# Optimization experiments

Measured on AMD Instinct MI355X. Metric: run time of the kernel, lower is better.

## Reference

```python
import jax, jax.numpy as jnp
import numpy as np

B, N, D = 4, 4096, 1024
H = 16
DH = D // H  # 64
SCALE = DH ** 0.5


def setup_inputs() -> dict:
    key = jax.random.key(0)
    ks = jax.random.split(key, 10)
    bound = float(np.sqrt(6.0 / (D + D)))  # xavier_uniform for square weights
    lin_b = float(1.0 / np.sqrt(D))        # default nn.Linear bias init bound
    return {
        "q": jax.random.normal(ks[0], (B, N, D), dtype=jnp.float32),
        "k": jax.random.normal(ks[1], (B, N, D), dtype=jnp.float32),
        "v": jax.random.normal(ks[2], (B, N, D), dtype=jnp.float32),
        "Wq": jax.random.uniform(ks[3], (D, D), jnp.float32, -bound, bound),
        "bq": jax.random.uniform(ks[4], (D,), jnp.float32, -lin_b, lin_b),
        "Wk": jax.random.uniform(ks[5], (D, D), jnp.float32, -bound, bound),
        "bk": jax.random.uniform(ks[6], (D,), jnp.float32, -lin_b, lin_b),
        "Wv": jax.random.uniform(ks[7], (D, D), jnp.float32, -bound, bound),
        "bv": jax.random.uniform(ks[8], (D,), jnp.float32, -lin_b, lin_b),
        "Wo": jax.random.uniform(ks[9], (D, D), jnp.float32, -bound, bound),
    }


def _split_heads(x):
    # [b, n, h*d] -> [b, h, n, d]
    b, n, _ = x.shape
    return x.reshape(b, n, H, DH).transpose(0, 2, 1, 3)


def reference(q, k, v, Wq, bq, Wk, bk, Wv, bv, Wo):
    qp = _split_heads(q @ Wq.T + bq)  # [b,h,n,d]
    kp = _split_heads(k @ Wk.T + bk)
    vp = _split_heads(v @ Wv.T + bv)

    inv_qtr = SCALE ** (-0.25)
    qs = jax.nn.softmax(qp, axis=-1) * inv_qtr            # feature-wise softmax on Q
    ctx = jnp.einsum('bhnd,bhne->bhde', kp, vp)           # K^T V: [b,h,d,d]
    ctx = jax.nn.softmax(ctx, axis=-2) * inv_qtr          # softmax over first d axis
    att = jnp.einsum('bhnd,bhde->bhne', qs, ctx)          # [b,h,n,d]

    att = att.transpose(0, 2, 1, 3).reshape(q.shape[0], q.shape[1], D)  # b n (h d)
    return att @ Wo.T  # to_out linear (no bias); dropout p=0 -> identity
```

## Files before the change

kernel.cpp:

```cpp
#include <hip/hip_runtime.h>

#define INV_QTR 0.59460355750136053f

typedef _Float16 f16;
typedef _Float16 f16x8 __attribute__((ext_vector_type(8)));
typedef float f32x4 __attribute__((ext_vector_type(4)));

__device__ __forceinline__ f16x8 load_cvt8(const float* p) {
    const f32x4* q = (const f32x4*)p;
    f32x4 a = q[0], b = q[1];
    f16x8 r;
    #pragma unroll
    for (int j = 0; j < 4; ++j) { r[j] = (f16)a[j]; r[j + 4] = (f16)b[j]; }
    return r;
}

template <bool XF, bool OF, bool BIAS>
__device__ __forceinline__ void gemm_bt_body(const void* __restrict__ X,
                                             const float* __restrict__ W,
                                             const float* __restrict__ bias,
                                             void* __restrict__ dst) {
    __shared__ __align__(16) f16 As[128 * 64];
    __shared__ __align__(16) f16 Bs[128 * 64];

    const int tid  = threadIdx.x;
    const int lane = tid & 63;
    const int wave = tid >> 6;
    const int m0   = blockIdx.x * 128;
    const int n0   = blockIdx.y * 128;
    const int wm   = (wave >> 1) * 64;
    const int wn   = (wave & 1) * 64;
    const int frow = lane & 15;
    const int quad = lane >> 4;

    f32x4 acc[4][4] = {};

    for (int k0 = 0; k0 < 1024; k0 += 64) {
        f16x8 stA[4], stB[4];
        #pragma unroll
        for (int i = 0; i < 4; ++i) {
            int slot = i * 256 + tid;
            int row  = slot >> 3;
            int sc   = slot & 7;
            int gc   = sc ^ (row & 7);
            size_t ax = (size_t)(m0 + row) * 1024 + k0 + gc * 8;
            if (XF) stA[i] = load_cvt8((const float*)X + ax);
            else    stA[i] = *(const f16x8*)((const f16*)X + ax);
            stB[i] = load_cvt8(W + (size_t)(n0 + row) * 1024 + k0 + gc * 8);
        }
        __syncthreads();
        #pragma unroll
        for (int i = 0; i < 4; ++i) {
            int slot = i * 256 + tid;
            *(f16x8*)(As + slot * 8) = stA[i];
            *(f16x8*)(Bs + slot * 8) = stB[i];
        }
        __syncthreads();

        #pragma unroll
        for (int kk = 0; kk < 2; ++kk) {
            f16x8 fa[4], fb[4];
            #pragma unroll
            for (int t = 0; t < 4; ++t) {
                int arow = wm + t * 16 + frow;
                int asc  = (kk * 4 + quad) ^ (arow & 7);
                fa[t] = *(const f16x8*)(As + arow * 64 + asc * 8);
                int brow = wn + t * 16 + frow;
                int bsc  = (kk * 4 + quad) ^ (brow & 7);
                fb[t] = *(const f16x8*)(Bs + brow * 64 + bsc * 8);
            }
            #pragma unroll
            for (int tm = 0; tm < 4; ++tm)
                #pragma unroll
                for (int tn = 0; tn < 4; ++tn)
                    acc[tm][tn] = __builtin_amdgcn_mfma_f32_16x16x32_f16(
                        fa[tm], fb[tn], acc[tm][tn], 0, 0, 0);
        }
    }

    #pragma unroll
    for (int tn = 0; tn < 4; ++tn) {
        int col = n0 + wn + tn * 16 + frow;
        float badd = BIAS ? bias[col] : 0.0f;
        #pragma unroll
        for (int tm = 0; tm < 4; ++tm) {
            #pragma unroll
            for (int r = 0; r < 4; ++r) {
                size_t idx = (size_t)(m0 + wm + tm * 16 + quad * 4 + r) * 1024 + col;
                float v = acc[tm][tn][r] + badd;
                if (OF) ((float*)dst)[idx] = v;
                else    ((f16*)dst)[idx] = (f16)v;
            }
        }
    }
}

__global__ void qkv_gemm(const float* __restrict__ q, const float* __restrict__ k,
                         const float* __restrict__ v,
                         const float* __restrict__ Wq, const float* __restrict__ bq,
                         const float* __restrict__ Wk, const float* __restrict__ bk,
                         const float* __restrict__ Wv, const float* __restrict__ bv,
                         f16* __restrict__ qp, f16* __restrict__ kp,
                         f16* __restrict__ vp) {
    int z = blockIdx.z;
    const float* X = (z == 0) ? q : (z == 1) ? k : v;
    const float* W = (z == 0) ? Wq : (z == 1) ? Wk : Wv;
    const float* bias = (z == 0) ? bq : (z == 1) ? bk : bv;
    f16* dst = (z == 0) ? qp : (z == 1) ? kp : vp;
    gemm_bt_body<true, false, true>(X, W, bias, dst);
}

__global__ void out_gemm(const f16* __restrict__ att, const float* __restrict__ Wo,
                         float* __restrict__ out) {
    gemm_bt_body<false, true, false>(att, Wo, nullptr, out);
}

__global__ void q_softmax(f16* __restrict__ qp) {
    int gid  = blockIdx.x * 4 + (threadIdx.x >> 6);
    int lane = threadIdx.x & 63;
    size_t off = (size_t)gid * 64 + lane;
    float x = (float)qp[off];
    float m = x;
    #pragma unroll
    for (int s = 32; s; s >>= 1) m = fmaxf(m, __shfl_xor(m, s, 64));
    float e = __expf(x - m);
    float sum = e;
    #pragma unroll
    for (int s = 32; s; s >>= 1) sum += __shfl_xor(sum, s, 64);
    qp[off] = (f16)(e / sum * INV_QTR);
}

__global__ void ctx_partial(const f16* __restrict__ kp, const f16* __restrict__ vp,
                            float* __restrict__ part) {
    int slice = blockIdx.x, bh = blockIdx.y;
    int b = bh >> 4, h = bh & 15;
    int tid = threadIdx.x, lane = tid & 63, wave = tid >> 6;
    __shared__ __align__(16) f16 kS[64 * 64];
    __shared__ __align__(16) f16 vS[64 * 64];

    const size_t base = ((size_t)b * 4096 + slice * 512) * 1024 + h * 64;
    const int dg = wave * 16;
    float acc[16] = {};

    for (int c = 0; c < 8; ++c) {
        f16x8 sk[2], sv[2];
        #pragma unroll
        for (int i = 0; i < 2; ++i) {
            int slot = i * 256 + tid, row = slot >> 3, ch = slot & 7;
            size_t g = base + (size_t)(c * 64 + row) * 1024 + ch * 8;
            sk[i] = *(const f16x8*)(kp + g);
            sv[i] = *(const f16x8*)(vp + g);
        }
        __syncthreads();
        #pragma unroll
        for (int i = 0; i < 2; ++i) {
            int slot = i * 256 + tid;
            *(f16x8*)(kS + slot * 8) = sk[i];
            *(f16x8*)(vS + slot * 8) = sv[i];
        }
        __syncthreads();
        #pragma unroll 4
        for (int n = 0; n < 64; ++n) {
            float vv = (float)vS[n * 64 + lane];
            f16x8 k0 = *(const f16x8*)(kS + n * 64 + dg);
            f16x8 k1 = *(const f16x8*)(kS + n * 64 + dg + 8);
            #pragma unroll
            for (int j = 0; j < 8; ++j) {
                acc[j]     += (float)k0[j] * vv;
                acc[8 + j] += (float)k1[j] * vv;
            }
        }
    }
    float* dst = part + ((size_t)(slice * 64 + bh) * 64 + dg) * 64 + lane;
    #pragma unroll
    for (int j = 0; j < 16; ++j) dst[j * 64] = acc[j];
}

__global__ void ctx_softmax(const float* __restrict__ part, f16* __restrict__ ctxT) {
    int bh = blockIdx.x;
    int tid = threadIdx.x;
    __shared__ float cs[64 * 65];
    float a[16];
    #pragma unroll
    for (int j = 0; j < 16; ++j) a[j] = 0.f;
    for (int s = 0; s < 8; ++s) {
        const float* p = part + (size_t)(s * 64 + bh) * 4096;
        #pragma unroll
        for (int j = 0; j < 16; ++j) a[j] += p[j * 256 + tid];
    }
    #pragma unroll
    for (int j = 0; j < 16; ++j) {
        int f = j * 256 + tid;
        cs[(f >> 6) * 65 + (f & 63)] = a[j];
    }
    __syncthreads();
    int lane = tid & 63, wave = tid >> 6;
    #pragma unroll
    for (int i = 0; i < 16; ++i) {
        int e = wave * 16 + i;
        float x = cs[lane * 65 + e];
        float m = x;
        #pragma unroll
        for (int s2 = 32; s2; s2 >>= 1) m = fmaxf(m, __shfl_xor(m, s2, 64));
        float ex = __expf(x - m);
        float sum = ex;
        #pragma unroll
        for (int s2 = 32; s2; s2 >>= 1) sum += __shfl_xor(sum, s2, 64);
        ctxT[((size_t)bh * 64 + e) * 64 + lane] = (f16)(ex / sum * INV_QTR);
    }
}

__global__ void att_gemm(const f16* __restrict__ qs, const f16* __restrict__ ctxT,
                         f16* __restrict__ att) {
    __shared__ __align__(16) f16 As[2][128 * 64];
    __shared__ __align__(16) f16 Bs[2][64 * 64];
    int tid = threadIdx.x, lane = tid & 63, wave = tid >> 6;
    int m0 = blockIdx.x * 128;
    int n0 = blockIdx.y * 128;
    int b  = m0 >> 12;
    int h0 = (n0 >> 6) & 15;

    #pragma unroll
    for (int ch = 0; ch < 2; ++ch) {
        #pragma unroll
        for (int i = 0; i < 4; ++i) {
            int slot = i * 256 + tid, row = slot >> 3, sc = slot & 7, gc = sc ^ (row & 7);
            *(f16x8*)(As[ch] + slot * 8) =
                *(const f16x8*)(qs + (size_t)(m0 + row) * 1024 + n0 + ch * 64 + gc * 8);
        }
        #pragma unroll
        for (int i = 0; i < 2; ++i) {
            int slot = i * 256 + tid, row = slot >> 3, sc = slot & 7, gc = sc ^ (row & 7);
            int bh = b * 16 + h0 + ch;
            *(f16x8*)(Bs[ch] + slot * 8) =
                *(const f16x8*)(ctxT + ((size_t)bh * 64 + row) * 64 + gc * 8);
        }
    }
    __syncthreads();

    int wm = (wave >> 1) * 64, wn = wave & 1;
    int frow = lane & 15, quad = lane >> 4;
    f32x4 acc[4][4] = {};
    #pragma unroll
    for (int kk = 0; kk < 2; ++kk) {
        f16x8 fa[4], fb[4];
        #pragma unroll
        for (int t = 0; t < 4; ++t) {
            int arow = wm + t * 16 + frow;
            int asc  = (kk * 4 + quad) ^ (arow & 7);
            fa[t] = *(const f16x8*)(As[wn] + arow * 64 + asc * 8);
            int brow = t * 16 + frow;
            int bsc  = (kk * 4 + quad) ^ (brow & 7);
            fb[t] = *(const f16x8*)(Bs[wn] + brow * 64 + bsc * 8);
        }
        #pragma unroll
        for (int tm = 0; tm < 4; ++tm)
            #pragma unroll
            for (int tn = 0; tn < 4; ++tn)
                acc[tm][tn] = __builtin_amdgcn_mfma_f32_16x16x32_f16(
                    fa[tm], fb[tn], acc[tm][tn], 0, 0, 0);
    }
    #pragma unroll
    for (int tn = 0; tn < 4; ++tn) {
        int col = n0 + wn * 64 + tn * 16 + frow;
        #pragma unroll
        for (int tm = 0; tm < 4; ++tm) {
            #pragma unroll
            for (int r = 0; r < 4; ++r) {
                int row = m0 + wm + tm * 16 + quad * 4 + r;
                att[(size_t)row * 1024 + col] = (f16)acc[tm][tn][r];
            }
        }
    }
}

extern "C" void kernel_launch(void* const* d_in, const int* in_sizes, int n_in,
                              void* d_out, int out_size, void* d_ws, size_t ws_size,
                              hipStream_t stream) {
    const float* q  = (const float*)d_in[0];
    const float* k  = (const float*)d_in[1];
    const float* v  = (const float*)d_in[2];
    const float* Wq = (const float*)d_in[3];
    const float* bq = (const float*)d_in[4];
    const float* Wk = (const float*)d_in[5];
    const float* bk = (const float*)d_in[6];
    const float* Wv = (const float*)d_in[7];
    const float* bv = (const float*)d_in[8];
    const float* Wo = (const float*)d_in[9];

    char* ws = (char*)d_ws;
    f16*   qp   = (f16*)ws;
    f16*   kp   = (f16*)(ws + 33554432);
    float* part = (float*)(ws + 67108864);
    f16*   ctxT = (f16*)(ws + 75497472);
    f16*   vp   = (f16*)d_out;
    float* out  = (float*)d_out;

    qkv_gemm<<<dim3(128, 8, 3), 256, 0, stream>>>(q, k, v, Wq, bq, Wk, bk, Wv, bv,
                                                  qp, kp, vp);
    q_softmax<<<65536, 256, 0, stream>>>(qp);
    ctx_partial<<<dim3(8, 64), 256, 0, stream>>>(kp, vp, part);
    ctx_softmax<<<64, 256, 0, stream>>>(part, ctxT);
    att_gemm<<<dim3(128, 8), 256, 0, stream>>>(qp, ctxT, kp);
    out_gemm<<<dim3(128, 8), 256, 0, stream>>>(kp, Wo, out);
}
```

Before: 589.5 us.

## Pre-convert inputs and weights to fp16 and load GEMM tiles directly into LDS

```diff
diff --git a/kernel.cpp b/kernel.cpp
--- a/kernel.cpp
+++ b/kernel.cpp
@@ -6,20 +6,45 @@
 typedef _Float16 f16x8 __attribute__((ext_vector_type(8)));
 typedef float f32x4 __attribute__((ext_vector_type(4)));
 
-__device__ __forceinline__ f16x8 load_cvt8(const float* p) {
-    const f32x4* q = (const f32x4*)p;
-    f32x4 a = q[0], b = q[1];
+__device__ __forceinline__ void gload16(const void* g, void* l) {
+    __builtin_amdgcn_global_load_lds(
+        (const __attribute__((address_space(1))) void*)g,
+        (__attribute__((address_space(3))) void*)l, 16, 0, 0);
+}
+
+__global__ void cvt_all(const float* __restrict__ q, const float* __restrict__ k,
+                        const float* __restrict__ v,
+                        const float* __restrict__ Wq, const float* __restrict__ Wk,
+                        const float* __restrict__ Wv, const float* __restrict__ Wo,
+                        f16* __restrict__ qh, f16* __restrict__ kh,
+                        f16* __restrict__ vh, f16* __restrict__ Wh) {
+    const long long NX = 16777216;
+    long long i = ((long long)blockIdx.x * 256 + threadIdx.x) * 8;
+    const float* src;
+    f16* dst;
+    if (i < NX)            { src = q + i;            dst = qh + i; }
+    else if (i < 2 * NX)   { src = k + (i - NX);     dst = kh + (i - NX); }
+    else if (i < 3 * NX)   { src = v + (i - 2 * NX); dst = vh + (i - 2 * NX); }
+    else {
+        long long wi = i - 3 * NX;
+        int wsel = (int)(wi >> 20);
+        const float* ws = (wsel == 0) ? Wq : (wsel == 1) ? Wk : (wsel == 2) ? Wv : Wo;
+        src = ws + (wi & 1048575);
+        dst = Wh + wi;
+    }
+    f32x4 a = ((const f32x4*)src)[0];
+    f32x4 b = ((const f32x4*)src)[1];
     f16x8 r;
     #pragma unroll
     for (int j = 0; j < 4; ++j) { r[j] = (f16)a[j]; r[j + 4] = (f16)b[j]; }
-    return r;
-}
-
-template <bool XF, bool OF, bool BIAS>
-__device__ __forceinline__ void gemm_bt_body(const void* __restrict__ X,
-                                             const float* __restrict__ W,
-                                             const float* __restrict__ bias,
-                                             void* __restrict__ dst) {
+    *(f16x8*)dst = r;
+}
+
+template <bool OF, bool BIAS>
+__device__ __forceinline__ void gemm_f16_body(const f16* __restrict__ X,
+                                              const f16* __restrict__ W,
+                                              const float* __restrict__ bias,
+                                              void* __restrict__ dst) {
     __shared__ __align__(16) f16 As[128 * 64];
     __shared__ __align__(16) f16 Bs[128 * 64];
 
@@ -36,24 +61,17 @@
     f32x4 acc[4][4] = {};
 
     for (int k0 = 0; k0 < 1024; k0 += 64) {
-        f16x8 stA[4], stB[4];
+        __syncthreads();
         #pragma unroll
         for (int i = 0; i < 4; ++i) {
             int slot = i * 256 + tid;
             int row  = slot >> 3;
             int sc   = slot & 7;
             int gc   = sc ^ (row & 7);
-            size_t ax = (size_t)(m0 + row) * 1024 + k0 + gc * 8;
-            if (XF) stA[i] = load_cvt8((const float*)X + ax);
-            else    stA[i] = *(const f16x8*)((const f16*)X + ax);
-            stB[i] = load_cvt8(W + (size_t)(n0 + row) * 1024 + k0 + gc * 8);
-        }
-        __syncthreads();
-        #pragma unroll
-        for (int i = 0; i < 4; ++i) {
-            int slot = i * 256 + tid;
-            *(f16x8*)(As + slot * 8) = stA[i];
-            *(f16x8*)(Bs + slot * 8) = stB[i];
+            gload16(X + (size_t)(m0 + row) * 1024 + k0 + gc * 8,
+                    (char*)As + slot * 16);
+            gload16(W + (size_t)(n0 + row) * 1024 + k0 + gc * 8,
+                    (char*)Bs + slot * 16);
         }
         __syncthreads();
 
@@ -95,24 +113,14 @@
     }
 }
 
-__global__ void qkv_gemm(const float* __restrict__ q, const float* __restrict__ k,
-                         const float* __restrict__ v,
-                         const float* __restrict__ Wq, const float* __restrict__ bq,
-                         const float* __restrict__ Wk, const float* __restrict__ bk,
-                         const float* __restrict__ Wv, const float* __restrict__ bv,
-                         f16* __restrict__ qp, f16* __restrict__ kp,
-                         f16* __restrict__ vp) {
-    int z = blockIdx.z;
-    const float* X = (z == 0) ? q : (z == 1) ? k : v;
-    const float* W = (z == 0) ? Wq : (z == 1) ? Wk : Wv;
-    const float* bias = (z == 0) ? bq : (z == 1) ? bk : bv;
-    f16* dst = (z == 0) ? qp : (z == 1) ? kp : vp;
-    gemm_bt_body<true, false, true>(X, W, bias, dst);
-}
-
-__global__ void out_gemm(const f16* __restrict__ att, const float* __restrict__ Wo,
+__global__ void proj_gemm(const f16* __restrict__ X, const f16* __restrict__ W,
+                          const float* __restrict__ bias, f16* __restrict__ dst) {
+    gemm_f16_body<false, true>(X, W, bias, dst);
+}
+
+__global__ void out_gemm(const f16* __restrict__ att, const f16* __restrict__ Wo,
                          float* __restrict__ out) {
-    gemm_bt_body<false, true, false>(att, Wo, nullptr, out);
+    gemm_f16_body<true, false>(att, Wo, nullptr, out);
 }
 
 __global__ void q_softmax(f16* __restrict__ qp) {
@@ -143,20 +151,13 @@
     float acc[16] = {};
 
     for (int c = 0; c < 8; ++c) {
-        f16x8 sk[2], sv[2];
+        __syncthreads();
         #pragma unroll
         for (int i = 0; i < 2; ++i) {
             int slot = i * 256 + tid, row = slot >> 3, ch = slot & 7;
             size_t g = base + (size_t)(c * 64 + row) * 1024 + ch * 8;
-            sk[i] = *(const f16x8*)(kp + g);
-            sv[i] = *(const f16x8*)(vp + g);
-        }
-        __syncthreads();
-        #pragma unroll
-        for (int i = 0; i < 2; ++i) {
-            int slot = i * 256 + tid;
-            *(f16x8*)(kS + slot * 8) = sk[i];
-            *(f16x8*)(vS + slot * 8) = sv[i];
+            gload16(kp + g, (char*)kS + slot * 16);
+            gload16(vp + g, (char*)vS + slot * 16);
         }
         __syncthreads();
         #pragma unroll 4
@@ -225,15 +226,15 @@
         #pragma unroll
         for (int i = 0; i < 4; ++i) {
             int slot = i * 256 + tid, row = slot >> 3, sc = slot & 7, gc = sc ^ (row & 7);
-            *(f16x8*)(As[ch] + slot * 8) =
-                *(const f16x8*)(qs + (size_t)(m0 + row) * 1024 + n0 + ch * 64 + gc * 8);
+            gload16(qs + (size_t)(m0 + row) * 1024 + n0 + ch * 64 + gc * 8,
+                    (char*)As[ch] + slot * 16);
         }
         #pragma unroll
         for (int i = 0; i < 2; ++i) {
             int slot = i * 256 + tid, row = slot >> 3, sc = slot & 7, gc = sc ^ (row & 7);
             int bh = b * 16 + h0 + ch;
-            *(f16x8*)(Bs[ch] + slot * 8) =
-                *(const f16x8*)(ctxT + ((size_t)bh * 64 + row) * 64 + gc * 8);
+            gload16(ctxT + ((size_t)bh * 64 + row) * 64 + gc * 8,
+                    (char*)Bs[ch] + slot * 16);
         }
     }
     __syncthreads();
@@ -289,18 +290,26 @@
     const float* Wo = (const float*)d_in[9];
 
     char* ws = (char*)d_ws;
-    f16*   qp   = (f16*)ws;
-    f16*   kp   = (f16*)(ws + 33554432);
-    float* part = (float*)(ws + 67108864);
+    char* ob = (char*)d_out;
+    f16*   vh   = (f16*)ws;
+    float* part = (float*)ws;
+    f16*   att  = (f16*)ws;
+    f16*   qp   = (f16*)(ws + 33554432);
+    f16*   Wh   = (f16*)(ws + 67108864);
     f16*   ctxT = (f16*)(ws + 75497472);
-    f16*   vp   = (f16*)d_out;
+    f16*   qh   = (f16*)ob;
+    f16*   kh   = (f16*)(ob + 33554432);
+    f16*   kp   = (f16*)ob;
+    f16*   vp   = (f16*)(ob + 33554432);
     float* out  = (float*)d_out;
 
-    qkv_gemm<<<dim3(128, 8, 3), 256, 0, stream>>>(q, k, v, Wq, bq, Wk, bk, Wv, bv,
-                                                  qp, kp, vp);
+    cvt_all<<<26624, 256, 0, stream>>>(q, k, v, Wq, Wk, Wv, Wo, qh, kh, vh, Wh);
+    proj_gemm<<<dim3(128, 8), 256, 0, stream>>>(qh, Wh,           bq, qp);
+    proj_gemm<<<dim3(128, 8), 256, 0, stream>>>(kh, Wh + 1048576, bk, kp);
+    proj_gemm<<<dim3(128, 8), 256, 0, stream>>>(vh, Wh + 2097152, bv, vp);
     q_softmax<<<65536, 256, 0, stream>>>(qp);
     ctx_partial<<<dim3(8, 64), 256, 0, stream>>>(kp, vp, part);
     ctx_softmax<<<64, 256, 0, stream>>>(part, ctxT);
-    att_gemm<<<dim3(128, 8), 256, 0, stream>>>(qp, ctxT, kp);
-    out_gemm<<<dim3(128, 8), 256, 0, stream>>>(kp, Wo, out);
-}
+    att_gemm<<<dim3(128, 8), 256, 0, stream>>>(qp, ctxT, att);
+    out_gemm<<<dim3(128, 8), 256, 0, stream>>>(att, Wh + 3145728, out);
+}
```

New measurement: 506.2 us. 14.1% less time.
